# Performance work log

Measured on AMD Instinct MI355X. Metric: run time of the kernel, lower is better.

The kernel has to match this reference:

```python
import jax, jax.numpy as jnp
import numpy as np

NUM_HEADS = 2
NUM_POINTS = 8
EMBED_DIM = 128


def conv2d(x, w, b, pad):
    # x: [B,C,H,W], w: [O,I,kh,kw]
    y = jax.lax.conv_general_dilated(
        x, w, window_strides=(1, 1), padding=[(pad, pad), (pad, pad)],
        dimension_numbers=('NCHW', 'OIHW', 'NCHW'))
    return y + b[None, :, None, None]


def grid_sample_bilinear(img, g):
    # img: [C,H,W]; g: [Ho,Wo,2] in [-1,1], (x, y) order; align_corners=False, zero padding
    C, H, W = img.shape
    x = ((g[..., 0] + 1.0) * W - 1.0) * 0.5
    y = ((g[..., 1] + 1.0) * H - 1.0) * 0.5
    x0 = jnp.floor(x); y0 = jnp.floor(y)
    x1 = x0 + 1.0; y1 = y0 + 1.0
    wx = x - x0; wy = y - y0

    def gather(yi, xi):
        valid = (xi >= 0) & (xi < W) & (yi >= 0) & (yi < H)
        xi_c = jnp.clip(xi, 0, W - 1).astype(jnp.int32)
        yi_c = jnp.clip(yi, 0, H - 1).astype(jnp.int32)
        v = img[:, yi_c, xi_c]  # [C,Ho,Wo]
        return v * valid[None].astype(img.dtype)

    out = (gather(y0, x0) * ((1 - wy) * (1 - wx))[None]
           + gather(y0, x1) * ((1 - wy) * wx)[None]
           + gather(y1, x0) * (wy * (1 - wx))[None]
           + gather(y1, x1) * (wy * wx)[None])
    return out  # [C,Ho,Wo]


def setup_inputs() -> dict:
    key = jax.random.key(0)
    ks = jax.random.split(key, 6)
    B, C, H, W = 8, EMBED_DIM, 96, 96
    query = jax.random.normal(ks[0], (B, C, H, W), dtype=jnp.float32)
    value = jax.random.normal(ks[1], (B, C, H, W), dtype=jnp.float32)
    reference_points = jax.random.uniform(ks[2], (B, H, W, NUM_HEADS, NUM_POINTS, 2), dtype=jnp.float32)
    attn_w = jax.random.normal(ks[3], (NUM_HEADS * NUM_POINTS, C, 3, 3), dtype=jnp.float32) * 0.05
    attn_b = jnp.zeros((NUM_HEADS * NUM_POINTS,), dtype=jnp.float32)
    proj_w = jax.random.normal(ks[4], (C, C, 1, 1), dtype=jnp.float32) * 0.05
    proj_b = jnp.zeros((C,), dtype=jnp.float32)
    return {"query": query, "value": value, "reference_points": reference_points,
            "attn_w": attn_w, "attn_b": attn_b, "proj_w": proj_w, "proj_b": proj_b}


def reference(query, value, reference_points, attn_w, attn_b, proj_w, proj_b):
    B, C, H, W = query.shape
    nh, npts = NUM_HEADS, NUM_POINTS
    hd = C // nh

    # attention weights: Conv2d(C, nh*np, 3, pad=1) -> softmax over points
    attn = conv2d(query, attn_w, attn_b, 1).reshape(B, nh, npts, H, W)
    attn = jax.nn.softmax(attn, axis=2)

    # grid: [B,H,W,nh,np,2] in [0,1] -> [-1,1] -> [B*nh, np, H, W, 2]
    grid = reference_points * 2.0 - 1.0
    grid = jnp.transpose(grid, (0, 3, 4, 1, 2, 5)).reshape(B * nh, npts, H, W, 2)

    # value per head: [B*nh, hd, H, W]
    val = value.reshape(B, nh, hd, H, W).reshape(B * nh, hd, H, W)

    # sample each point from the shared per-head value map (no materialized expand)
    sample_pts = jax.vmap(grid_sample_bilinear, in_axes=(None, 0))   # over points
    sampled = jax.vmap(sample_pts, in_axes=(0, 0))(val, grid)        # [B*nh, np, hd, H, W]
    sampled = sampled.reshape(B, nh, npts, hd, H, W)

    # weighted sum over points
    weighted = jnp.einsum('bnphw,bnpdhw->bndhw', attn, sampled).reshape(B, C, H, W)

    return conv2d(weighted, proj_w, proj_b, 0)
```

## Files before the change

### kernel.cpp

```cpp
#include <hip/hip_runtime.h>
#include <hip/hip_bf16.h>

#define BB 8
#define CC 128
#define HH 96
#define WW 96
#define HWH (HH*WW)
#define NH 2
#define NP 8
#define PW 98
#define PHW (PW*PW)

typedef __attribute__((ext_vector_type(8))) short short8;
typedef __attribute__((ext_vector_type(4))) float f32x4;

__global__ __launch_bounds__(256) void prep_w_kernel(
    const float* __restrict__ aw, const float* __restrict__ pw,
    __hip_bfloat16* __restrict__ wtb, float* __restrict__ pwT) {
  int t = blockIdx.x * 256 + threadIdx.x;
  for (int idx = t; idx < 9 * 16 * 16 * 8; idx += gridDim.x * 256) {
    int j = idx & 7;
    int o = (idx >> 3) & 15;
    int g = (idx >> 7) & 15;
    int k = idx >> 11;
    int c = g * 8 + j;
    wtb[idx] = __float2bfloat16(aw[o * 1152 + c * 9 + k]);
  }
  for (int idx = t; idx < 128 * 128; idx += gridDim.x * 256) {
    int co = idx & 127;
    int ci = idx >> 7;
    pwT[ci * 128 + co] = pw[co * 128 + ci];
  }
}

__global__ __launch_bounds__(256) void transpose_cl_kernel(
    const float* __restrict__ value, const float* __restrict__ query,
    __hip_bfloat16* __restrict__ val_t, __hip_bfloat16* __restrict__ q_pad) {
  __shared__ float tile[64][65];
  int blk = blockIdx.x;
  int mode = blk / 2304;
  int r = blk % 2304;
  int ptile = r % 144;
  int bn = r / 144;
  int b = bn >> 1, n = bn & 1;
  int pix0 = ptile * 64;
  int t = threadIdx.x;
  int lane = t & 63;
  int row4 = t >> 6;

  const float* srcp = (mode ? query : value) + ((size_t)(b * CC + n * 64)) * HWH + pix0;
#pragma unroll
  for (int i = 0; i < 16; ++i) {
    int c = i * 4 + row4;
    tile[c][lane] = srcp[(size_t)c * HWH + lane];
  }
  __syncthreads();

  int d2 = t & 31;
  int ph = t >> 5;
  if (mode == 0) {
    __hip_bfloat16* dst = val_t + ((size_t)bn * HWH + pix0) * 64;
#pragma unroll
    for (int i = 0; i < 8; ++i) {
      int p = i * 8 + ph;
      __hip_bfloat162 v;
      v.x = __float2bfloat16(tile[d2 * 2][p]);
      v.y = __float2bfloat16(tile[d2 * 2 + 1][p]);
      *reinterpret_cast<__hip_bfloat162*>(dst + (size_t)p * 64 + d2 * 2) = v;
    }
  } else {
#pragma unroll
    for (int i = 0; i < 8; ++i) {
      int p = i * 8 + ph;
      int gp = pix0 + p;
      int h = gp / WW, w = gp - h * WW;
      __hip_bfloat162 v;
      v.x = __float2bfloat16(tile[d2 * 2][p]);
      v.y = __float2bfloat16(tile[d2 * 2 + 1][p]);
      size_t off = ((size_t)b * PHW + (size_t)(h + 1) * PW + (w + 1)) * 128 + n * 64 + d2 * 2;
      *reinterpret_cast<__hip_bfloat162*>(q_pad + off) = v;
    }
  }
}

__global__ __launch_bounds__(256) void attn_conv_mfma2(
    const __hip_bfloat16* __restrict__ q_pad, const __hip_bfloat16* __restrict__ wtb_,
    const float* __restrict__ bias, float* __restrict__ attn_out) {
  int t = threadIdx.x;
  int l = t & 63;
  int bid = blockIdx.x;
  int sbid = (bid & 7) * 144 + (bid >> 3);
  int tid = __builtin_amdgcn_readfirstlane(sbid * 4 + (t >> 6));
  int b = tid / 576;
  int rem = tid % 576;
  int h = rem / 6;
  int w0 = (rem % 6) * 16;

  const char* qb = (const char*)q_pad;
  const char* wb = (const char*)wtb_;

  int pxbase = b * PHW + (h + 1) * PW + (w0 + 1);
  int lb  = (l & 15) * 256 + (l >> 4) * 16;
  int wlb = (l >> 4) * 256 + (l & 15) * 16;

  float bias_o = bias[l & 15];
  f32x4 acc0 = {bias_o, bias_o, bias_o, bias_o};
  f32x4 acc1 = {0.f, 0.f, 0.f, 0.f};

#pragma unroll
  for (int k = 0; k < 9; ++k) {
    int dy = k / 3 - 1, dx = (k % 3) - 1;
    const char* abase = qb + ((size_t)pxbase + dy * PW + dx) * 256 + lb;
    const char* bbase = wb + k * 4096 + wlb;
#pragma unroll
    for (int c4 = 0; c4 < 4; ++c4) {
      short8 a = *(const short8*)(abase + c4 * 64);
      short8 bf = *(const short8*)(bbase + c4 * 1024);
      if (k & 1)
        acc1 = __builtin_amdgcn_mfma_f32_16x16x32_bf16(a, bf, acc1, 0, 0, 0);
      else
        acc0 = __builtin_amdgcn_mfma_f32_16x16x32_bf16(a, bf, acc0, 0, 0, 0);
    }
  }

  int o = l & 15;
  size_t row0 = (size_t)b * HWH + (size_t)h * 96 + w0 + (l >> 4) * 4;
#pragma unroll
  for (int r = 0; r < 4; ++r) {
    float vv = acc0[r] + acc1[r];
    float mx = vv;
    mx = fmaxf(mx, __shfl_xor(mx, 1, 64));
    mx = fmaxf(mx, __shfl_xor(mx, 2, 64));
    mx = fmaxf(mx, __shfl_xor(mx, 4, 64));
    float e = __expf(vv - mx);
    float s = e;
    s += __shfl_xor(s, 1, 64);
    s += __shfl_xor(s, 2, 64);
    s += __shfl_xor(s, 4, 64);
    attn_out[(row0 + r) * 16 + o] = e / s;
  }
}

__global__ __launch_bounds__(256) void sample_kernel(
    const __hip_bfloat16* __restrict__ val_t, const float* __restrict__ attn,
    const float* __restrict__ refp, __hip_bfloat16* __restrict__ weighted) {
  int t = threadIdx.x;
  int lane = t & 63;
  int bid = blockIdx.x;
  int sbid = (bid & 7) * (36864 / 8) + (bid >> 3);
  int wid = __builtin_amdgcn_readfirstlane(sbid * 4 + (t >> 6));
  int bn = wid / HWH;
  int pix = wid % HWH;
  int b = bn >> 1, n = bn & 1;

  const float* ap = attn + (size_t)(b * HWH + pix) * 16 + n * 8;
  const float* rp = refp + ((size_t)(b * HWH + pix) * NH + n) * 16;
  const __hip_bfloat16* vb = val_t + (size_t)bn * HWH * 64;

  float4 a0 = *(const float4*)(ap);
  float4 a1 = *(const float4*)(ap + 4);
  float4 r0 = *(const float4*)(rp);
  float4 r1 = *(const float4*)(rp + 4);
  float4 r2 = *(const float4*)(rp + 8);
  float4 r3 = *(const float4*)(rp + 12);
  float aa[8] = {a0.x, a0.y, a0.z, a0.w, a1.x, a1.y, a1.z, a1.w};
  float rr[16] = {r0.x, r0.y, r0.z, r0.w, r1.x, r1.y, r1.z, r1.w,
                  r2.x, r2.y, r2.z, r2.w, r3.x, r3.y, r3.z, r3.w};

  float acc = 0.f;
#pragma unroll
  for (int p = 0; p < 8; ++p) {
    float a = aa[p];
    float x = rr[p * 2 + 0] * (float)WW - 0.5f;
    float y = rr[p * 2 + 1] * (float)HH - 0.5f;
    float x0f = floorf(x), y0f = floorf(y);
    float wx = x - x0f, wy = y - y0f;
    int x0 = (int)x0f, y0 = (int)y0f;

    float vx0 = (x0 >= 0) ? 1.f : 0.f;
    float vx1 = (x0 < WW - 1) ? 1.f : 0.f;
    float vy0 = (y0 >= 0) ? 1.f : 0.f;
    float vy1 = (y0 < HH - 1) ? 1.f : 0.f;

    int xc0 = max(x0, 0), xc1 = min(x0 + 1, WW - 1);
    int yc0 = max(y0, 0), yc1 = min(y0 + 1, HH - 1);

    float v00 = __bfloat162float(vb[((size_t)yc0 * WW + xc0) * 64 + lane]);
    float v01 = __bfloat162float(vb[((size_t)yc0 * WW + xc1) * 64 + lane]);
    float v10 = __bfloat162float(vb[((size_t)yc1 * WW + xc0) * 64 + lane]);
    float v11 = __bfloat162float(vb[((size_t)yc1 * WW + xc1) * 64 + lane]);

    float w00 = a * (1.f - wy) * (1.f - wx) * vy0 * vx0;
    float w01 = a * (1.f - wy) * wx * vy0 * vx1;
    float w10 = a * wy * (1.f - wx) * vy1 * vx0;
    float w11 = a * wy * wx * vy1 * vx1;

    acc = fmaf(v00, w00, acc);
    acc = fmaf(v01, w01, acc);
    acc = fmaf(v10, w10, acc);
    acc = fmaf(v11, w11, acc);
  }
  weighted[((size_t)b * HWH + pix) * 128 + n * 64 + lane] = __float2bfloat16(acc);
}

__global__ __launch_bounds__(256) void proj_kernel(
    const __hip_bfloat16* __restrict__ weighted, const float* __restrict__ pwT,
    const float* __restrict__ pb, float* __restrict__ out) {
  __shared__ float A[64][129];
  int t = threadIdx.x;
  int pix0 = blockIdx.x * 64;

  const ushort4* src = reinterpret_cast<const ushort4*>(weighted + (size_t)pix0 * 128);
#pragma unroll
  for (int i = 0; i < 8; ++i) {
    int idx = i * 256 + t;
    ushort4 v = src[idx];
    int row = idx >> 5;
    int col = (idx & 31) * 4;
    A[row][col + 0] = __bfloat162float(*reinterpret_cast<__hip_bfloat16*>(&v.x));
    A[row][col + 1] = __bfloat162float(*reinterpret_cast<__hip_bfloat16*>(&v.y));
    A[row][col + 2] = __bfloat162float(*reinterpret_cast<__hip_bfloat16*>(&v.z));
    A[row][col + 3] = __bfloat162float(*reinterpret_cast<__hip_bfloat16*>(&v.w));
  }
  __syncthreads();

  int lane = t & 63;
  int g = __builtin_amdgcn_readfirstlane(t >> 6);

  float acc[32];
  const float* pbg = pb + g * 32;
#pragma unroll
  for (int j = 0; j < 32; ++j) acc[j] = pbg[j];

  const float* pwt_g = pwT + g * 32;
  for (int ci = 0; ci < 128; ++ci) {
    float a = A[lane][ci];
    const float* row = pwt_g + (size_t)ci * 128;
#pragma unroll
    for (int j = 0; j < 32; ++j) acc[j] = fmaf(a, row[j], acc[j]);
  }

  int gp = pix0 + lane;
  int b = gp / HWH;
  int pixl = gp % HWH;
  float* ob = out + ((size_t)b * CC + g * 32) * HWH + pixl;
#pragma unroll
  for (int j = 0; j < 32; ++j) ob[(size_t)j * HWH] = acc[j];
}

extern "C" void kernel_launch(void* const* d_in, const int* in_sizes, int n_in,
                              void* d_out, int out_size, void* d_ws, size_t ws_size,
                              hipStream_t stream) {
  const float* query = (const float*)d_in[0];
  const float* value = (const float*)d_in[1];
  const float* refp  = (const float*)d_in[2];
  const float* aw    = (const float*)d_in[3];
  const float* ab    = (const float*)d_in[4];
  const float* pw    = (const float*)d_in[5];
  const float* pb    = (const float*)d_in[6];
  float* out = (float*)d_out;

  char* ws = (char*)d_ws;
  __hip_bfloat16* wtb      = (__hip_bfloat16*)(ws);
  float* pwT               = (float*)(ws + 40960);
  float* attn_sm           = (float*)(ws + 106496);
  __hip_bfloat16* val_t    = (__hip_bfloat16*)(ws + 4825088);
  __hip_bfloat16* q_pad    = (__hip_bfloat16*)(ws + 23699456);
  __hip_bfloat16* weighted = (__hip_bfloat16*)(ws + 23699456);

  hipMemsetAsync(q_pad, 0, (size_t)BB * PHW * 128 * 2, stream);
  prep_w_kernel<<<72, 256, 0, stream>>>(aw, pw, wtb, pwT);
  transpose_cl_kernel<<<4608, 256, 0, stream>>>(value, query, val_t, q_pad);
  attn_conv_mfma2<<<1152, 256, 0, stream>>>(q_pad, wtb, ab, attn_sm);
  sample_kernel<<<(BB * NH * HWH) / 4, 256, 0, stream>>>(val_t, attn_sm, refp, weighted);
  proj_kernel<<<(BB * HWH) / 64, 256, 0, stream>>>(weighted, pwT, pb, out);
}
```

Baseline: 286.0 us.

## Process four pixels per wavefront with vectorized 4-channel bf16 gathers in sampler

The sampling kernel now assigns a 16-lane quarter-wave to each (batch, head, pixel) unit. Each lane handles 4 channels through 8-byte uint2 loads and bit-shift bf16 unpacking, and stores a packed ushort4. This cuts the grid to a quarter and lowers instruction count per gathered value, targeting gather and issue overhead. Per-lane attention and reference-point loads now differ within a wave instead of being uniform scalar loads, which may add vector memory traffic.

```diff
diff --git a/kernel.cpp b/kernel.cpp
--- a/kernel.cpp
+++ b/kernel.cpp
@@ -13,6 +13,9 @@
 
 typedef __attribute__((ext_vector_type(8))) short short8;
 typedef __attribute__((ext_vector_type(4))) float f32x4;
+
+__device__ __forceinline__ float bf_lo(unsigned u) { return __uint_as_float(u << 16); }
+__device__ __forceinline__ float bf_hi(unsigned u) { return __uint_as_float(u & 0xffff0000u); }
 
 __global__ __launch_bounds__(256) void prep_w_kernel(
     const float* __restrict__ aw, const float* __restrict__ pw,
@@ -146,16 +149,18 @@
     const float* __restrict__ refp, __hip_bfloat16* __restrict__ weighted) {
   int t = threadIdx.x;
   int lane = t & 63;
+  int sub = lane >> 4;
+  int lq = lane & 15;
   int bid = blockIdx.x;
-  int sbid = (bid & 7) * (36864 / 8) + (bid >> 3);
-  int wid = __builtin_amdgcn_readfirstlane(sbid * 4 + (t >> 6));
-  int bn = wid / HWH;
-  int pix = wid % HWH;
-  int b = bn >> 1, n = bn & 1;
-
-  const float* ap = attn + (size_t)(b * HWH + pix) * 16 + n * 8;
-  const float* rp = refp + ((size_t)(b * HWH + pix) * NH + n) * 16;
-  const __hip_bfloat16* vb = val_t + (size_t)bn * HWH * 64;
+  int sbid = (bid & 7) * 1152 + (bid >> 3);
+  int unit = (sbid * 4 + (t >> 6)) * 4 + sub;
+  int bn = unit / HWH;
+  int pix = unit - bn * HWH;
+  int bq = bn >> 1, n = bn & 1;
+
+  const float* ap = attn + ((size_t)bq * HWH + pix) * 16 + n * 8;
+  const float* rp = refp + (((size_t)bq * HWH + pix) * NH + n) * 16;
+  const __hip_bfloat16* vb = val_t + (size_t)bn * (HWH * 64);
 
   float4 a0 = *(const float4*)(ap);
   float4 a1 = *(const float4*)(ap + 4);
@@ -167,7 +172,8 @@
   float rr[16] = {r0.x, r0.y, r0.z, r0.w, r1.x, r1.y, r1.z, r1.w,
                   r2.x, r2.y, r2.z, r2.w, r3.x, r3.y, r3.z, r3.w};
 
-  float acc = 0.f;
+  float acc0 = 0.f, acc1 = 0.f, acc2 = 0.f, acc3 = 0.f;
+  int lq4 = lq * 4;
 #pragma unroll
   for (int p = 0; p < 8; ++p) {
     float a = aa[p];
@@ -177,30 +183,58 @@
     float wx = x - x0f, wy = y - y0f;
     int x0 = (int)x0f, y0 = (int)y0f;
 
-    float vx0 = (x0 >= 0) ? 1.f : 0.f;
-    float vx1 = (x0 < WW - 1) ? 1.f : 0.f;
-    float vy0 = (y0 >= 0) ? 1.f : 0.f;
-    float vy1 = (y0 < HH - 1) ? 1.f : 0.f;
+    float ay0 = a * (1.f - wy);  ay0 = (y0 >= 0)      ? ay0 : 0.f;
+    float ay1 = a * wy;          ay1 = (y0 < HH - 1)  ? ay1 : 0.f;
+    float bx0 = 1.f - wx;        bx0 = (x0 >= 0)      ? bx0 : 0.f;
+    float bx1 = wx;              bx1 = (x0 < WW - 1)  ? bx1 : 0.f;
 
     int xc0 = max(x0, 0), xc1 = min(x0 + 1, WW - 1);
     int yc0 = max(y0, 0), yc1 = min(y0 + 1, HH - 1);
 
-    float v00 = __bfloat162float(vb[((size_t)yc0 * WW + xc0) * 64 + lane]);
-    float v01 = __bfloat162float(vb[((size_t)yc0 * WW + xc1) * 64 + lane]);
-    float v10 = __bfloat162float(vb[((size_t)yc1 * WW + xc0) * 64 + lane]);
-    float v11 = __bfloat162float(vb[((size_t)yc1 * WW + xc1) * 64 + lane]);
-
-    float w00 = a * (1.f - wy) * (1.f - wx) * vy0 * vx0;
-    float w01 = a * (1.f - wy) * wx * vy0 * vx1;
-    float w10 = a * wy * (1.f - wx) * vy1 * vx0;
-    float w11 = a * wy * wx * vy1 * vx1;
-
-    acc = fmaf(v00, w00, acc);
-    acc = fmaf(v01, w01, acc);
-    acc = fmaf(v10, w10, acc);
-    acc = fmaf(v11, w11, acc);
-  }
-  weighted[((size_t)b * HWH + pix) * 128 + n * 64 + lane] = __float2bfloat16(acc);
+    int r0o = yc0 * (WW * 64);
+    int r1o = yc1 * (WW * 64);
+    int c0o = xc0 * 64 + lq4;
+    int c1o = xc1 * 64 + lq4;
+
+    const uint2* p00 = (const uint2*)(vb + (r0o + c0o));
+    const uint2* p01 = (const uint2*)(vb + (r0o + c1o));
+    const uint2* p10 = (const uint2*)(vb + (r1o + c0o));
+    const uint2* p11 = (const uint2*)(vb + (r1o + c1o));
+    uint2 u00 = *p00, u01 = *p01, u10 = *p10, u11 = *p11;
+
+    float w00 = ay0 * bx0, w01 = ay0 * bx1, w10 = ay1 * bx0, w11 = ay1 * bx1;
+
+    acc0 = fmaf(bf_lo(u00.x), w00, acc0);
+    acc1 = fmaf(bf_hi(u00.x), w00, acc1);
+    acc2 = fmaf(bf_lo(u00.y), w00, acc2);
+    acc3 = fmaf(bf_hi(u00.y), w00, acc3);
+
+    acc0 = fmaf(bf_lo(u01.x), w01, acc0);
+    acc1 = fmaf(bf_hi(u01.x), w01, acc1);
+    acc2 = fmaf(bf_lo(u01.y), w01, acc2);
+    acc3 = fmaf(bf_hi(u01.y), w01, acc3);
+
+    acc0 = fmaf(bf_lo(u10.x), w10, acc0);
+    acc1 = fmaf(bf_hi(u10.x), w10, acc1);
+    acc2 = fmaf(bf_lo(u10.y), w10, acc2);
+    acc3 = fmaf(bf_hi(u10.y), w10, acc3);
+
+    acc0 = fmaf(bf_lo(u11.x), w11, acc0);
+    acc1 = fmaf(bf_hi(u11.x), w11, acc1);
+    acc2 = fmaf(bf_lo(u11.y), w11, acc2);
+    acc3 = fmaf(bf_hi(u11.y), w11, acc3);
+  }
+
+  ushort4 outv;
+  __hip_bfloat16 h0 = __float2bfloat16(acc0);
+  __hip_bfloat16 h1 = __float2bfloat16(acc1);
+  __hip_bfloat16 h2 = __float2bfloat16(acc2);
+  __hip_bfloat16 h3 = __float2bfloat16(acc3);
+  outv.x = *(unsigned short*)&h0;
+  outv.y = *(unsigned short*)&h1;
+  outv.z = *(unsigned short*)&h2;
+  outv.w = *(unsigned short*)&h3;
+  *(ushort4*)(weighted + ((size_t)bq * HWH + pix) * 128 + n * 64 + lq4) = outv;
 }
 
 __global__ __launch_bounds__(256) void proj_kernel(
@@ -272,6 +306,6 @@
   prep_w_kernel<<<72, 256, 0, stream>>>(aw, pw, wtb, pwT);
   transpose_cl_kernel<<<4608, 256, 0, stream>>>(value, query, val_t, q_pad);
   attn_conv_mfma2<<<1152, 256, 0, stream>>>(q_pad, wtb, ab, attn_sm);
-  sample_kernel<<<(BB * NH * HWH) / 4, 256, 0, stream>>>(val_t, attn_sm, refp, weighted);
+  sample_kernel<<<9216, 256, 0, stream>>>(val_t, attn_sm, refp, weighted);
   proj_kernel<<<(BB * HWH) / 64, 256, 0, stream>>>(weighted, pwT, pb, out);
 }
```

After: 256.9 us. 10.2% less time.
